# Kernel optimization log

Measured on AMD Instinct MI355X. Metric: run time of the kernel, lower is better.

## Reference

```python
import jax, jax.numpy as jnp
import numpy as np

MAX_LEN = 2048
D_MODEL = 1024
NUM_HEADS = 16
D_HEAD = D_MODEL // NUM_HEADS
BATCH = 2
SEQ = 2048


def setup_inputs() -> dict:
    key = jax.random.key(0)
    ks = jax.random.split(key, 8)
    scale = 1.0 / np.sqrt(D_MODEL)
    return {
        "x": jax.random.normal(ks[0], (BATCH, SEQ, D_MODEL), dtype=jnp.float32),
        "Wq": jax.random.normal(ks[1], (D_MODEL, D_MODEL), dtype=jnp.float32) * scale,
        "bq": jnp.zeros((D_MODEL,), dtype=jnp.float32),
        "Wk": jax.random.normal(ks[2], (D_MODEL, D_MODEL), dtype=jnp.float32) * scale,
        "bk": jnp.zeros((D_MODEL,), dtype=jnp.float32),
        "Wv": jax.random.normal(ks[3], (D_MODEL, D_MODEL), dtype=jnp.float32) * scale,
        "bv": jnp.zeros((D_MODEL,), dtype=jnp.float32),
        "Er": jax.random.normal(ks[4], (MAX_LEN, D_HEAD), dtype=jnp.float32),
    }


def _skew(QEr):
    # QEr: [B, H, S, S] -> Transformer-XL skew -> Srel: [B, H, S, S]
    B, H, S, _ = QEr.shape
    padded = jnp.pad(QEr, ((0, 0), (0, 0), (0, 0), (1, 0)))  # [B,H,S,S+1]
    reshaped = padded.reshape(B, H, S + 1, S)
    return reshaped[:, :, 1:, :]


def reference(x, Wq, bq, Wk, bk, Wv, bv, Er):
    B, S, D = x.shape
    H, dh = NUM_HEADS, D // NUM_HEADS
    q = (x @ Wq + bq).reshape(B, S, H, dh).transpose(0, 2, 1, 3)  # [B,H,S,dh]
    k = (x @ Wk + bk).reshape(B, S, H, dh).transpose(0, 2, 1, 3)
    v = (x @ Wv + bv).reshape(B, S, H, dh).transpose(0, 2, 1, 3)
    Er_s = Er[MAX_LEN - S:, :]                                    # [S, dh]
    QEr = jnp.einsum("bhsd,ld->bhsl", q, Er_s)                    # [B,H,S,S]
    Srel = _skew(QEr)
    QKt = jnp.einsum("bhsd,bhtd->bhst", q, k)
    attn = (QKt + Srel) / jnp.sqrt(jnp.asarray(dh, x.dtype))
    causal = jnp.tril(jnp.ones((S, S), dtype=bool))
    attn = jnp.where(causal[None, None], attn, -jnp.inf)
    attn = jax.nn.softmax(attn, axis=-1)
    out = jnp.einsum("bhst,bhtd->bhsd", attn, v)                  # [B,H,S,dh]
    return out.transpose(0, 2, 1, 3).reshape(B, S, D)             # dropout in eval = identity
```

## Files before the change

kernel.cpp:

```cpp
#include <hip/hip_runtime.h>
#include <hip/hip_bf16.h>

#define SLEN   2048
#define DMODEL 1024
#define NHEADS 16
#define DHEAD  64
#define NBATCH 2
#define EPAD_ROWS 2432

#define QSCALE 0.18033688011112042f
#define EXPB   23.083120654223414f

typedef __bf16 bf16x8 __attribute__((ext_vector_type(8)));
typedef float  f32x4  __attribute__((ext_vector_type(4)));

__device__ __forceinline__ unsigned short f2bf(float f) {
    unsigned int u = __builtin_bit_cast(unsigned int, f);
    return (unsigned short)((u + 0x7fffu + ((u >> 16) & 1u)) >> 16);
}

__device__ __forceinline__ float exp2_hw(float x) {
    float r;
    asm("v_exp_f32 %0, %1" : "=v"(r) : "v"(x));
    return r;
}

__device__ __forceinline__ unsigned int cvtpk_bf16(float lo, float hi) {
    unsigned int d;
    asm("v_cvt_pk_bf16_f32 %0, %1, %2" : "=v"(d) : "v"(lo), "v"(hi));
    return d;
}

__device__ __forceinline__ bf16x8 ld8(const unsigned short* p) {
    union { uint4 u; bf16x8 b; } t;
    t.u = *(const uint4*)p;
    return t.b;
}

__device__ __forceinline__ void glds16(const unsigned short* g, unsigned short* l) {
    __builtin_amdgcn_global_load_lds(
        (const __attribute__((address_space(1))) unsigned int*)g,
        (__attribute__((address_space(3))) unsigned int*)l, 16, 0, 0);
}

__global__ __launch_bounds__(256) void prep_kernel(
    const float* __restrict__ x, const float* __restrict__ Er,
    const float* __restrict__ Wq, const float* __restrict__ Wk,
    const float* __restrict__ Wv,
    unsigned short* __restrict__ xb, unsigned short* __restrict__ Ep,
    unsigned short* __restrict__ Wt) {
    const int bi = blockIdx.x, tid = threadIdx.x;
    if (bi < 4096) {
        int i = (bi * 256 + tid) * 4;
        float4 v = *(const float4*)(x + i);
        ushort4 o;
        o.x = f2bf(v.x); o.y = f2bf(v.y); o.z = f2bf(v.z); o.w = f2bf(v.w);
        *(ushort4*)(xb + i) = o;
    } else if (bi < 4704) {
        int i = (bi - 4096) * 256 + tid;
        int row = i >> 6;
        unsigned short v = 0;
        if (row < SLEN) v = f2bf(Er[i]);
        Ep[i] = v;
    } else {
        __shared__ float tile[32][33];
        const int b3 = bi - 4704;
        const int z = b3 >> 10, rem = b3 & 1023;
        const int n0 = (rem & 31) * 32, k0 = (rem >> 5) * 32;
        const float* W = (z == 0) ? Wq : (z == 1 ? Wk : Wv);
        unsigned short* out = Wt + (size_t)z * DMODEL * DMODEL;
        const int tx = tid & 31, ty = tid >> 5;
        for (int r = 0; r < 32; r += 8)
            tile[ty + r][tx] = W[(size_t)(k0 + ty + r) * DMODEL + n0 + tx];
        __syncthreads();
        for (int r = 0; r < 32; r += 8)
            out[(size_t)(n0 + ty + r) * DMODEL + k0 + tx] = f2bf(tile[tx][ty + r]);
    }
}

__global__ __launch_bounds__(256, 2) void qkv_gemm(
    const unsigned short* __restrict__ xb, const unsigned short* __restrict__ Wt,
    const float* __restrict__ bq, const float* __restrict__ bk, const float* __restrict__ bv,
    unsigned short* __restrict__ Qs, unsigned short* __restrict__ Ks,
    unsigned short* __restrict__ Vts) {
    const int b = blockIdx.x;
    const int mt = b & 31, nt = b >> 5;
    const int m0 = mt * 128, n0 = nt * 64;

    __shared__ __align__(16) unsigned short As[128][64];
    __shared__ __align__(16) unsigned short Bs[3][64][64];

    const int tid = threadIdx.x;
    const int wave = tid >> 6, lane = tid & 63, l16 = lane & 15, quad = lane >> 4;
    const int wm = (wave >> 1) * 64, wn2 = (wave & 1) * 32;

    const int lr8 = lane >> 3;
    const int sc  = ((lane & 7) ^ lr8) * 8;

    f32x4 accQ[4][2], accK[4][2], accV[2][4];
#pragma unroll
    for (int mi = 0; mi < 4; mi++)
#pragma unroll
        for (int ni = 0; ni < 2; ni++) {
            accQ[mi][ni] = (f32x4){0.f, 0.f, 0.f, 0.f};
            accK[mi][ni] = (f32x4){0.f, 0.f, 0.f, 0.f};
            accV[ni][mi] = (f32x4){0.f, 0.f, 0.f, 0.f};
        }

    for (int j = 0; j < 16; ++j) {
        if (j) __syncthreads();
        const int k0 = j * 64;
#pragma unroll
        for (int c = 0; c < 4; c++) {
            const int seg = wave * 4 + c;
            glds16(&xb[(size_t)(m0 + seg * 8 + lr8) * DMODEL + k0 + sc], &As[seg * 8][0]);
        }
#pragma unroll
        for (int c = 0; c < 6; c++) {
            const int idx = wave * 6 + c;
            const int z = idx >> 3, seg = idx & 7;
            glds16(&Wt[(size_t)z * DMODEL * DMODEL + (size_t)(n0 + seg * 8 + lr8) * DMODEL + k0 + sc],
                   &Bs[z][seg * 8][0]);
        }
        __syncthreads();

#pragma unroll
        for (int ks = 0; ks < 2; ks++) {
            const int pc = ((ks * 4 + quad) ^ (l16 & 7)) * 8;
            bf16x8 a[4], bb[3][2];
#pragma unroll
            for (int mi = 0; mi < 4; mi++) a[mi] = ld8(&As[wm + mi * 16 + l16][pc]);
#pragma unroll
            for (int z = 0; z < 3; z++)
#pragma unroll
                for (int ni = 0; ni < 2; ni++) bb[z][ni] = ld8(&Bs[z][wn2 + ni * 16 + l16][pc]);
#pragma unroll
            for (int mi = 0; mi < 4; mi++)
#pragma unroll
                for (int ni = 0; ni < 2; ni++) {
                    accQ[mi][ni] = __builtin_amdgcn_mfma_f32_16x16x32_bf16(a[mi], bb[0][ni], accQ[mi][ni], 0, 0, 0);
                    accK[mi][ni] = __builtin_amdgcn_mfma_f32_16x16x32_bf16(a[mi], bb[1][ni], accK[mi][ni], 0, 0, 0);
                    accV[ni][mi] = __builtin_amdgcn_mfma_f32_16x16x32_bf16(bb[2][ni], a[mi], accV[ni][mi], 0, 0, 0);
                }
        }
    }

    const int hh = n0 >> 6;

#pragma unroll
    for (int ni = 0; ni < 2; ni++) {
        const int n = n0 + wn2 + ni * 16 + l16;
        const float bqv = bq[n], bkv = bk[n];
        const int d = n & 63;
#pragma unroll
        for (int mi = 0; mi < 4; mi++)
#pragma unroll
            for (int r = 0; r < 4; r++) {
                const int m = m0 + wm + mi * 16 + quad * 4 + r;
                const int bi = m >> 11, s = m & 2047;
                Qs[((size_t)(bi * NHEADS + hh) * SLEN + s) * 64 + d] =
                    f2bf((accQ[mi][ni][r] + bqv) * QSCALE);
                Ks[((size_t)(bi * NHEADS + hh) * SLEN + s) * 64 + d] =
                    f2bf(accK[mi][ni][r] + bkv);
            }
    }
#pragma unroll
    for (int ni = 0; ni < 2; ni++)
#pragma unroll
        for (int r = 0; r < 4; r++) {
            const int n = n0 + wn2 + ni * 16 + quad * 4 + r;
            const float bvv = bv[n];
            const int d = n & 63;
#pragma unroll
            for (int mi = 0; mi < 4; mi++) {
                const int m = m0 + wm + mi * 16 + l16;
                const int bi = m >> 11, s = m & 2047;
                Vts[((size_t)((bi * NHEADS + hh) * 64 + d)) * SLEN + s] =
                    f2bf(accV[ni][mi][r] + bvv);
            }
        }
}

__global__ __launch_bounds__(256, 3) void attn_kernel(
    const unsigned short* __restrict__ Q,
    const unsigned short* __restrict__ K,
    const unsigned short* __restrict__ Vt,
    const unsigned short* __restrict__ Ep,
    float* __restrict__ out) {
    const int tid = threadIdx.x;
    const int wave = tid >> 6, lane = tid & 63, l16 = lane & 15, quad = lane >> 4;
    const int lr8 = lane >> 3;
    const int swz = ((lane & 7) ^ lr8) * 8;

    const int bh = blockIdx.x & 31;
    const int qt = 31 - (blockIdx.x >> 5);
    const int s0 = qt * 64;
    const int ntp = qt + 1;

    __shared__ __align__(16) unsigned short Ksh[64 * 64];
    __shared__ __align__(16) unsigned short Vsh[2][64 * 64];
    __shared__ __align__(16) unsigned short Esh[192 * 64];

    const unsigned short* Qb = Q + (size_t)bh * SLEN * 64;
    const unsigned short* Kb = K + (size_t)bh * SLEN * 64;
    const unsigned short* Vb = Vt + (size_t)bh * 64 * SLEN;
    const int ob = bh >> 4, oh = bh & 15;

    const int pc0 = (quad ^ (l16 & 7)) * 8;
    const int pc1 = ((4 + quad) ^ (l16 & 7)) * 8;
    const int krot = (15 - l16) & 3;
    const bool c1 = (krot & 1) != 0, c2 = (krot & 2) != 0;
    int permE[4]; bool hiE[4];
#pragma unroll
    for (int r = 0; r < 4; r++) {
        const int idx = quad * 4 + r + 15 - l16;
        permE[r] = ((idx >> 2) & 3) * 16 + l16;
        const int c  = r + 15 - l16;
        const int qv = (quad - (c >> 2)) & 3;
        hiE[r] = (qv * 4 + c) >= 16;
    }

    const int sw = s0 + 16 * wave;
    const bf16x8 aq0 = ld8(Qb + (size_t)(sw + l16) * 64 + quad * 8);
    const bf16x8 aq1 = ld8(Qb + (size_t)(sw + l16) * 64 + 32 + quad * 8);

    f32x4 accO[4];
    float sacc[4];
#pragma unroll
    for (int nt = 0; nt < 4; nt++) accO[nt] = (f32x4){0.f, 0.f, 0.f, 0.f};
#pragma unroll
    for (int r = 0; r < 4; r++) sacc[r] = 0.f;

    const int p0row = SLEN - 64 - s0;

#pragma unroll
    for (int c = 0; c < 2; c++) {
        const int seg = wave * 2 + c;
        glds16(&Kb[(size_t)(seg * 8 + lr8) * 64 + swz], &Ksh[seg * 8 * 64]);
        glds16(&Vb[(size_t)(seg * 8 + lr8) * SLEN + swz], &Vsh[0][seg * 8 * 64]);
    }
#pragma unroll
    for (int u = 0; u < 4; u++) {
        const int idx = wave * 4 + u;
        glds16(&Ep[(size_t)(p0row + idx * 8 + lr8) * 64 + swz], &Esh[idx * 8 * 64]);
    }
    __syncthreads();

    f32x4 carryE = (f32x4){0.f, 0.f, 0.f, 0.f};
    int rb = 48 - 16 * wave;
    int ed = 128;

    for (int j = 0; j < ntp; ++j) {
        const int t0 = j * 64;
        const int cur = j & 1;

        f32x4 accS[4];
#pragma unroll
        for (int nt = 0; nt < 4; nt++)
            accS[nt] = (f32x4){-EXPB, -EXPB, -EXPB, -EXPB};
#pragma unroll
        for (int nt = 0; nt < 4; nt++) {
            bf16x8 bk0 = ld8(&Ksh[(nt * 16 + l16) * 64 + pc0]);
            bf16x8 bk1 = ld8(&Ksh[(nt * 16 + l16) * 64 + pc1]);
            accS[nt] = __builtin_amdgcn_mfma_f32_16x16x32_bf16(bk0, aq0, accS[nt], 0, 0, 0);
            accS[nt] = __builtin_amdgcn_mfma_f32_16x16x32_bf16(bk1, aq1, accS[nt], 0, 0, 0);
        }

        __syncthreads();

        if (j + 1 < ntp) {
            const int t1 = t0 + 64, nb = cur ^ 1;
#pragma unroll
            for (int c = 0; c < 2; c++) {
                const int seg = wave * 2 + c;
                glds16(&Kb[(size_t)(t1 + seg * 8 + lr8) * 64 + swz], &Ksh[seg * 8 * 64]);
                glds16(&Vb[(size_t)(seg * 8 + lr8) * SLEN + t1 + swz], &Vsh[nb][seg * 8 * 64]);
            }
            const int er = p0row + t0 + 128;
#pragma unroll
            for (int c = 0; c < 2; c++) {
                const int seg = wave * 2 + c;
                glds16(&Ep[(size_t)(er + seg * 8 + lr8) * 64 + swz],
                       &Esh[(ed + seg * 8) * 64]);
            }
        }

        const int base = rb + l16;
        f32x4 accE[5];
        if (j == 0) {
            accE[0] = (f32x4){0.f, 0.f, 0.f, 0.f};
            bf16x8 be0 = ld8(&Esh[base * 64 + pc0]);
            bf16x8 be1 = ld8(&Esh[base * 64 + pc1]);
            accE[0] = __builtin_amdgcn_mfma_f32_16x16x32_bf16(be0, aq0, accE[0], 0, 0, 0);
            accE[0] = __builtin_amdgcn_mfma_f32_16x16x32_bf16(be1, aq1, accE[0], 0, 0, 0);
        } else {
            accE[0] = carryE;
        }
#pragma unroll
        for (int nt = 1; nt < 5; nt++) {
            int row = base + nt * 16;
            if (row >= 192) row -= 192;
            accE[nt] = (f32x4){0.f, 0.f, 0.f, 0.f};
            bf16x8 be0 = ld8(&Esh[row * 64 + pc0]);
            bf16x8 be1 = ld8(&Esh[row * 64 + pc1]);
            accE[nt] = __builtin_amdgcn_mfma_f32_16x16x32_bf16(be0, aq0, accE[nt], 0, 0, 0);
            accE[nt] = __builtin_amdgcn_mfma_f32_16x16x32_bf16(be1, aq1, accE[nt], 0, 0, 0);
        }
        carryE = accE[4];
        rb += 64; if (rb >= 192) rb -= 192;
        ed += 64; if (ed >= 192) ed -= 192;

        f32x4 rotE[5];
#pragma unroll
        for (int g = 0; g < 5; g++) {
            f32x4 A = accE[g], t, rt;
#pragma unroll
            for (int r = 0; r < 4; r++) t[r] = c1 ? A[(r + 1) & 3] : A[r];
#pragma unroll
            for (int r = 0; r < 4; r++) rt[r] = c2 ? t[(r + 2) & 3] : t[r];
            rotE[g] = rt;
        }

        float pe[4][4];
        auto scoreblk = [&](bool masked) {
#pragma unroll
            for (int nt = 0; nt < 4; nt++) {
#pragma unroll
                for (int r = 0; r < 4; r++) {
                    float send = hiE[r] ? rotE[nt + 1][r] : rotE[nt][r];
                    float rel = __shfl(send, permE[r]);
                    float p = exp2_hw(accS[nt][r] + rel);
                    if (masked)
                        p = (t0 + nt * 16 + quad * 4 + r <= sw + l16) ? p : 0.0f;
                    sacc[r] += p;
                    pe[nt][r] = p;
                }
            }
        };
        if (t0 + 63 <= sw) scoreblk(false);
        else               scoreblk(true);

        unsigned int w[4][2];
#pragma unroll
        for (int nt = 0; nt < 4; nt++) {
            w[nt][0] = cvtpk_bf16(pe[nt][0], pe[nt][1]);
            w[nt][1] = cvtpk_bf16(pe[nt][2], pe[nt][3]);
        }
        bf16x8 pf[2];
#pragma unroll
        for (int c = 0; c < 2; c++) {
            unsigned int a0 = w[2 * c][0], b0 = w[2 * c + 1][0];
            unsigned int a1 = w[2 * c][1], b1 = w[2 * c + 1][1];
            asm volatile("v_permlane32_swap_b32 %0, %1" : "+v"(a0), "+v"(b0));
            asm volatile("v_permlane16_swap_b32 %0, %1" : "+v"(a0), "+v"(b0));
            asm volatile("v_permlane32_swap_b32 %0, %1" : "+v"(a1), "+v"(b1));
            asm volatile("v_permlane16_swap_b32 %0, %1" : "+v"(a1), "+v"(b1));
            union { uint4 u; bf16x8 b; } t;
            t.u = (uint4){a0, a1, b0, b1};
            pf[c] = t.b;
        }

#pragma unroll
        for (int ntd = 0; ntd < 4; ntd++) {
            bf16x8 bv0 = ld8(&Vsh[cur][(ntd * 16 + l16) * 64 + pc0]);
            bf16x8 bv1 = ld8(&Vsh[cur][(ntd * 16 + l16) * 64 + pc1]);
            accO[ntd] = __builtin_amdgcn_mfma_f32_16x16x32_bf16(bv0, pf[0], accO[ntd], 0, 0, 0);
            accO[ntd] = __builtin_amdgcn_mfma_f32_16x16x32_bf16(bv1, pf[1], accO[ntd], 0, 0, 0);
        }

        __syncthreads();
    }

    float s4 = (sacc[0] + sacc[1]) + (sacc[2] + sacc[3]);
    s4 += __shfl_xor(s4, 16);
    s4 += __shfl_xor(s4, 32);
    const float inv = 1.f / s4;
    const int srow = sw + l16;
    float* orow = out + ((size_t)(ob * SLEN + srow)) * DMODEL + oh * 64 + quad * 4;
#pragma unroll
    for (int ntd = 0; ntd < 4; ntd++) {
        float4 st = {accO[ntd][0] * inv, accO[ntd][1] * inv,
                     accO[ntd][2] * inv, accO[ntd][3] * inv};
        *(float4*)(orow + ntd * 16) = st;
    }
}

extern "C" void kernel_launch(void* const* d_in, const int* in_sizes, int n_in,
                              void* d_out, int out_size, void* d_ws, size_t ws_size,
                              hipStream_t stream) {
    const float* x  = (const float*)d_in[0];
    const float* Wq = (const float*)d_in[1];
    const float* bq = (const float*)d_in[2];
    const float* Wk = (const float*)d_in[3];
    const float* bk = (const float*)d_in[4];
    const float* Wv = (const float*)d_in[5];
    const float* bv = (const float*)d_in[6];
    const float* Er = (const float*)d_in[7];
    float* out = (float*)d_out;

    char* p = (char*)d_ws;
    unsigned short* xb  = (unsigned short*)p; p += (size_t)4096 * 1024 * 2;
    unsigned short* Wt  = (unsigned short*)p; p += (size_t)3 * 1024 * 1024 * 2;
    unsigned short* Qs  = (unsigned short*)p; p += (size_t)32 * 2048 * 64 * 2;
    unsigned short* Ks  = (unsigned short*)p; p += (size_t)32 * 2048 * 64 * 2;
    unsigned short* Vts = (unsigned short*)p; p += (size_t)32 * 2048 * 64 * 2;
    unsigned short* Ep  = (unsigned short*)p; p += (size_t)EPAD_ROWS * 64 * 2;

    hipLaunchKernelGGL(prep_kernel, dim3(7776), dim3(256), 0, stream,
                       x, Er, Wq, Wk, Wv, xb, Ep, Wt);
    hipLaunchKernelGGL(qkv_gemm, dim3(512), dim3(256), 0, stream,
                       xb, Wt, bq, bk, bv, Qs, Ks, Vts);
    hipLaunchKernelGGL(attn_kernel, dim3(1024), dim3(256), 0, stream, Qs, Ks, Vts, Ep, out);
}
```

Before: 168.8 us.

## Raise attention occupancy, single-buffer V, pack shuffles to fp16, reorder tiles

The attention kernel's V shared buffer goes from double to single, so LDS use per block drops, and launch bounds now target 4 blocks per SIMD instead of 3. The V tile load now starts at the top of each iteration rather than being prefetched a full step ahead. The relative-position shuffle packs two values as fp16 into one lane shuffle, halving cross-lane traffic at some cost in precision. Block-to-query-tile mapping is reordered in a zigzag of four groups to balance causal work across waves of blocks. The risks are exposed V load latency, register pressure under the tighter launch bound, and fp16 rounding error on the relative terms.

```diff
diff --git a/kernel.cpp b/kernel.cpp
--- a/kernel.cpp
+++ b/kernel.cpp
@@ -13,6 +13,7 @@
 
 typedef __bf16 bf16x8 __attribute__((ext_vector_type(8)));
 typedef float  f32x4  __attribute__((ext_vector_type(4)));
+typedef __fp16 hf16x2 __attribute__((ext_vector_type(2)));
 
 __device__ __forceinline__ unsigned short f2bf(float f) {
     unsigned int u = __builtin_bit_cast(unsigned int, f);
@@ -29,6 +30,15 @@
     unsigned int d;
     asm("v_cvt_pk_bf16_f32 %0, %1, %2" : "=v"(d) : "v"(lo), "v"(hi));
     return d;
+}
+
+__device__ __forceinline__ unsigned int pkf16(float a, float b) {
+    hf16x2 h = __builtin_amdgcn_cvt_pkrtz(a, b);
+    return __builtin_bit_cast(unsigned int, h);
+}
+__device__ __forceinline__ void unpkf16(unsigned int u, float& lo, float& hi) {
+    hf16x2 h = __builtin_bit_cast(hf16x2, u);
+    lo = (float)h[0]; hi = (float)h[1];
 }
 
 __device__ __forceinline__ bf16x8 ld8(const unsigned short* p) {
@@ -181,7 +191,7 @@
         }
 }
 
-__global__ __launch_bounds__(256, 3) void attn_kernel(
+__global__ __launch_bounds__(256, 4) void attn_kernel(
     const unsigned short* __restrict__ Q,
     const unsigned short* __restrict__ K,
     const unsigned short* __restrict__ Vt,
@@ -192,13 +202,16 @@
     const int lr8 = lane >> 3;
     const int swz = ((lane & 7) ^ lr8) * 8;
 
-    const int bh = blockIdx.x & 31;
-    const int qt = 31 - (blockIdx.x >> 5);
+    const int b = blockIdx.x;
+    const int g = b >> 8, ii = b & 255, tsl = ii >> 5;
+    const int bh = ii & 31;
+    const int qt = (g == 0) ? (31 - tsl) : (g == 1) ? (16 + tsl)
+                 : (g == 2) ? (15 - tsl) : tsl;
     const int s0 = qt * 64;
     const int ntp = qt + 1;
 
     __shared__ __align__(16) unsigned short Ksh[64 * 64];
-    __shared__ __align__(16) unsigned short Vsh[2][64 * 64];
+    __shared__ __align__(16) unsigned short Vsh[64 * 64];
     __shared__ __align__(16) unsigned short Esh[192 * 64];
 
     const unsigned short* Qb = Q + (size_t)bh * SLEN * 64;
@@ -237,7 +250,7 @@
     for (int c = 0; c < 2; c++) {
         const int seg = wave * 2 + c;
         glds16(&Kb[(size_t)(seg * 8 + lr8) * 64 + swz], &Ksh[seg * 8 * 64]);
-        glds16(&Vb[(size_t)(seg * 8 + lr8) * SLEN + swz], &Vsh[0][seg * 8 * 64]);
+        glds16(&Vb[(size_t)(seg * 8 + lr8) * SLEN + swz], &Vsh[seg * 8 * 64]);
     }
 #pragma unroll
     for (int u = 0; u < 4; u++) {
@@ -252,7 +265,14 @@
 
     for (int j = 0; j < ntp; ++j) {
         const int t0 = j * 64;
-        const int cur = j & 1;
+
+        if (j > 0) {
+#pragma unroll
+            for (int c = 0; c < 2; c++) {
+                const int seg = wave * 2 + c;
+                glds16(&Vb[(size_t)(seg * 8 + lr8) * SLEN + t0 + swz], &Vsh[seg * 8 * 64]);
+            }
+        }
 
         f32x4 accS[4];
 #pragma unroll
@@ -269,12 +289,11 @@
         __syncthreads();
 
         if (j + 1 < ntp) {
-            const int t1 = t0 + 64, nb = cur ^ 1;
+            const int t1 = t0 + 64;
 #pragma unroll
             for (int c = 0; c < 2; c++) {
                 const int seg = wave * 2 + c;
                 glds16(&Kb[(size_t)(t1 + seg * 8 + lr8) * 64 + swz], &Ksh[seg * 8 * 64]);
-                glds16(&Vb[(size_t)(seg * 8 + lr8) * SLEN + t1 + swz], &Vsh[nb][seg * 8 * 64]);
             }
             const int er = p0row + t0 + 128;
 #pragma unroll
@@ -312,28 +331,36 @@
 
         f32x4 rotE[5];
 #pragma unroll
-        for (int g = 0; g < 5; g++) {
-            f32x4 A = accE[g], t, rt;
+        for (int gg = 0; gg < 5; gg++) {
+            f32x4 A = accE[gg], t, rt;
 #pragma unroll
             for (int r = 0; r < 4; r++) t[r] = c1 ? A[(r + 1) & 3] : A[r];
 #pragma unroll
             for (int r = 0; r < 4; r++) rt[r] = c2 ? t[(r + 2) & 3] : t[r];
-            rotE[g] = rt;
+            rotE[gg] = rt;
         }
 
         float pe[4][4];
         auto scoreblk = [&](bool masked) {
 #pragma unroll
-            for (int nt = 0; nt < 4; nt++) {
+            for (int p = 0; p < 2; p++) {
 #pragma unroll
                 for (int r = 0; r < 4; r++) {
-                    float send = hiE[r] ? rotE[nt + 1][r] : rotE[nt][r];
-                    float rel = __shfl(send, permE[r]);
-                    float p = exp2_hw(accS[nt][r] + rel);
-                    if (masked)
-                        p = (t0 + nt * 16 + quad * 4 + r <= sw + l16) ? p : 0.0f;
-                    sacc[r] += p;
-                    pe[nt][r] = p;
+                    float s0v = hiE[r] ? rotE[2 * p + 1][r] : rotE[2 * p][r];
+                    float s1v = hiE[r] ? rotE[2 * p + 2][r] : rotE[2 * p + 1][r];
+                    unsigned int pk = pkf16(s0v, s1v);
+                    unsigned int got = (unsigned int)__shfl((int)pk, permE[r]);
+                    float rel0, rel1;
+                    unpkf16(got, rel0, rel1);
+                    float p0 = exp2_hw(accS[2 * p][r] + rel0);
+                    float p1 = exp2_hw(accS[2 * p + 1][r] + rel1);
+                    if (masked) {
+                        p0 = (t0 + (2 * p) * 16 + quad * 4 + r <= sw + l16) ? p0 : 0.0f;
+                        p1 = (t0 + (2 * p + 1) * 16 + quad * 4 + r <= sw + l16) ? p1 : 0.0f;
+                    }
+                    sacc[r] += p0 + p1;
+                    pe[2 * p][r] = p0;
+                    pe[2 * p + 1][r] = p1;
                 }
             }
         };
@@ -362,8 +389,8 @@
 
 #pragma unroll
         for (int ntd = 0; ntd < 4; ntd++) {
-            bf16x8 bv0 = ld8(&Vsh[cur][(ntd * 16 + l16) * 64 + pc0]);
-            bf16x8 bv1 = ld8(&Vsh[cur][(ntd * 16 + l16) * 64 + pc1]);
+            bf16x8 bv0 = ld8(&Vsh[(ntd * 16 + l16) * 64 + pc0]);
+            bf16x8 bv1 = ld8(&Vsh[(ntd * 16 + l16) * 64 + pc1]);
             accO[ntd] = __builtin_amdgcn_mfma_f32_16x16x32_bf16(bv0, pf[0], accO[ntd], 0, 0, 0);
             accO[ntd] = __builtin_amdgcn_mfma_f32_16x16x32_bf16(bv1, pf[1], accO[ntd], 0, 0, 0);
         }
```

Result: no change. 171.9 us (+1.8%).
